# Kernel tuning notes

Measured on AMD Instinct MI355X. Metric: run time of the kernel, lower is better.

Reference implementation:

```python
import jax, jax.numpy as jnp
import numpy as np

D_MODEL = 1024
NUM_HEADS = 16
D_HEAD = D_MODEL // NUM_HEADS
THETA = 10000.0


def _rope_tables(seq_len, d_k, theta):
    # inv_powers_k = theta**(-(2k-2)/d_k) for k=1..d_k/2 == theta**(-arange(0,d_k,2)/d_k)
    inv_powers = theta ** (-jnp.arange(0, d_k, 2, dtype=jnp.float32) / d_k)  # [d_k/2]
    positions = jnp.arange(seq_len, dtype=jnp.float32)
    angles = jnp.outer(positions, inv_powers)  # [S, d_k/2]
    return jnp.cos(angles), jnp.sin(angles)


def _apply_rope(x, cos, sin):
    # x: [..., S, d_k]; cos/sin: [S, d_k/2] broadcast over leading dims
    x_even = x[..., 0::2]
    x_odd = x[..., 1::2]
    r_even = x_even * cos - x_odd * sin
    r_odd = x_even * sin + x_odd * cos
    # interleave back: [..., S, d_k/2, 2] -> [..., S, d_k]
    return jnp.stack([r_even, r_odd], axis=-1).reshape(x.shape)


def setup_inputs() -> dict:
    key = jax.random.key(0)
    ks = jax.random.split(key, 5)
    B, S = 2, 2048
    sigma = (2.0 / (D_MODEL + D_MODEL)) ** 0.5
    x = jax.random.normal(ks[0], (B, S, D_MODEL), dtype=jnp.float32)
    wq = jax.random.normal(ks[1], (D_MODEL, D_MODEL), dtype=jnp.float32) * sigma
    wk = jax.random.normal(ks[2], (D_MODEL, D_MODEL), dtype=jnp.float32) * sigma
    wv = jax.random.normal(ks[3], (D_MODEL, D_MODEL), dtype=jnp.float32) * sigma
    wo = jax.random.normal(ks[4], (D_MODEL, D_MODEL), dtype=jnp.float32) * sigma
    return {"x": x, "wq": wq, "wk": wk, "wv": wv, "wo": wo}


def reference(x, wq, wk, wv, wo):
    B, S, D = x.shape
    H, Dh = NUM_HEADS, D_HEAD
    # Linear: einx.dot('... in, out in -> ... out') == x @ W.T
    q = jnp.einsum('bsd,od->bso', x, wq)
    k = jnp.einsum('bsd,od->bso', x, wk)
    v = jnp.einsum('bsd,od->bso', x, wv)
    # split heads: [B, S, H, Dh] -> [B, H, S, Dh]
    q = q.reshape(B, S, H, Dh).transpose(0, 2, 1, 3)
    k = k.reshape(B, S, H, Dh).transpose(0, 2, 1, 3)
    v = v.reshape(B, S, H, Dh).transpose(0, 2, 1, 3)
    cos, sin = _rope_tables(S, Dh, THETA)
    q = _apply_rope(q, cos, sin)
    k = _apply_rope(k, cos, sin)
    scale = 1.0 / jnp.sqrt(jnp.float32(Dh))
    scores = jnp.einsum('bhqd,bhkd->bhqk', q, k) * scale  # [B,H,S,S]
    causal = jnp.tril(jnp.ones((S, S), dtype=bool))
    scores = jnp.where(causal, scores, -jnp.inf)
    probs = jax.nn.softmax(scores, axis=-1)
    attn = jnp.einsum('bhqk,bhkd->bhqd', probs, v)
    attn = attn.transpose(0, 2, 1, 3).reshape(B, S, D)
    return jnp.einsum('bsd,od->bso', attn, wo)
```

## Files before the change

### kernel.cpp

```cpp
#include <hip/hip_runtime.h>
#include <hip/hip_bf16.h>
#include <math.h>

#define B_SZ   2
#define SEQ    2048
#define DM     1024
#define NH     16
#define DH     64
#define MROWS  (B_SZ * SEQ)
#define DQKV   (3 * DM)

typedef __attribute__((ext_vector_type(8))) short short8;
typedef __attribute__((ext_vector_type(4))) float f32x4;
typedef __attribute__((ext_vector_type(4))) unsigned short us4;
typedef __attribute__((ext_vector_type(2))) unsigned int u32x2;

__device__ __forceinline__ float b2f(unsigned short u) {
    union { float f; unsigned int i; } x; x.i = ((unsigned int)u) << 16; return x.f;
}
__device__ __forceinline__ unsigned short f2b(float f) {
    union { float f; unsigned int i; } x; x.f = f;
    return (unsigned short)((x.i + 0x7fffu + ((x.i >> 16) & 1u)) >> 16);
}
__device__ __forceinline__ unsigned int pk2b(float a, float b) {
    float2 f2; f2.x = a; f2.y = b;
    __hip_bfloat162 hb = __float22bfloat162_rn(f2);
    return *reinterpret_cast<unsigned int*>(&hb);
}

__device__ __forceinline__ void gload_lds16(const unsigned short* g, unsigned short* lds_base_uniform) {
    __builtin_amdgcn_global_load_lds(
        (const __attribute__((address_space(1))) unsigned int*)g,
        (__attribute__((address_space(3))) unsigned int*)lds_base_uniform,
        16, 0, 0);
}

#define NX4 (MROWS * DM / 4)
#define NW4 (DM * DM / 4)

__global__ __launch_bounds__(256) void cvt_all(const float* __restrict__ x,
                                               const float* __restrict__ wq,
                                               const float* __restrict__ wk,
                                               const float* __restrict__ wv,
                                               const float* __restrict__ wo,
                                               unsigned short* __restrict__ xb,
                                               unsigned short* __restrict__ wqkv,
                                               unsigned short* __restrict__ wob,
                                               float* __restrict__ tab) {
    const int i = blockIdx.x * 256 + threadIdx.x;
    const int ncvt = NX4 + 4 * NW4;
    if (i < ncvt) {
        const float* src; unsigned short* dst; int off;
        if (i < NX4) { src = x; dst = xb; off = i; }
        else {
            int j = i - NX4;
            int w = j >> 18;
            off = j & (NW4 - 1);
            src = (w == 0) ? wq : (w == 1) ? wk : (w == 2) ? wv : wo;
            dst = (w < 3) ? wqkv + (size_t)w * DM * DM : wob;
        }
        float4 v = reinterpret_cast<const float4*>(src)[off];
        us4 o = { f2b(v.x), f2b(v.y), f2b(v.z), f2b(v.w) };
        reinterpret_cast<us4*>(dst)[off] = o;
    } else {
        int t = i - ncvt;
        if (t < SEQ * 32) {
            int s = t >> 5, fi = t & 31;
            float inv = powf(10000.0f, -(float)fi / 32.0f);
            float ang = (float)s * inv;
            tab[2 * t]     = cosf(ang);
            tab[2 * t + 1] = sinf(ang);
        }
    }
}

#define BM 128
#define BN 128
#define BK 32

__global__ __launch_bounds__(256, 2) void gemm_out(const unsigned short* __restrict__ A,
                                                   const unsigned short* __restrict__ B,
                                                   float* __restrict__ Cout) {
    const int OBM = 128, OBN = 64;
    __shared__ unsigned short As[2][OBM * BK];
    __shared__ unsigned short Bs[2][OBN * BK];
    const int tid  = threadIdx.x;
    const int lane = tid & 63, wid = tid >> 6;
    const int lm = lane & 15, lg = lane >> 4;
    const int brow = blockIdx.y * OBM, bcol = blockIdx.x * OBN;
    const int K = DM, N = DM;

    f32x4 acc[2][4] = {};

    const int rA  = tid >> 2;
    const int kc8 = (tid & 3) * 8;
    const unsigned short* gA0 = A + (size_t)(brow + rA) * K + kc8;
    const unsigned short* gA1 = A + (size_t)(brow + 64 + rA) * K + kc8;
    const unsigned short* gB0 = B + (size_t)(bcol + rA) * K + kc8;
    unsigned short* lA0 = (unsigned short*)As + wid * 512;
    unsigned short* lA1 = (unsigned short*)As + 2048 + wid * 512;
    unsigned short* lB0 = (unsigned short*)Bs + wid * 512;

    gload_lds16(gA0, lA0);
    gload_lds16(gA1, lA1);
    gload_lds16(gB0, lB0);
    __syncthreads();

    int buf = 0;
    for (int k0 = 0; k0 < K; k0 += BK) {
        if (k0 + BK < K) {
            gload_lds16(gA0 + k0 + BK, lA0 + (buf ^ 1) * 4096);
            gload_lds16(gA1 + k0 + BK, lA1 + (buf ^ 1) * 4096);
            gload_lds16(gB0 + k0 + BK, lB0 + (buf ^ 1) * 2048);
        }
        short8 a[2], b[4];
#pragma unroll
        for (int m = 0; m < 2; ++m)
            a[m] = *reinterpret_cast<const short8*>(&As[buf][(wid * 32 + m * 16 + lm) * BK + lg * 8]);
#pragma unroll
        for (int n = 0; n < 4; ++n)
            b[n] = *reinterpret_cast<const short8*>(&Bs[buf][(n * 16 + lm) * BK + lg * 8]);
#pragma unroll
        for (int m = 0; m < 2; ++m)
#pragma unroll
            for (int n = 0; n < 4; ++n)
                acc[m][n] = __builtin_amdgcn_mfma_f32_16x16x32_bf16(a[m], b[n], acc[m][n], 0, 0, 0);
        __syncthreads();
        buf ^= 1;
    }

#pragma unroll
    for (int m = 0; m < 2; ++m) {
#pragma unroll
        for (int r = 0; r < 4; ++r) {
            const size_t base = (size_t)(brow + wid * 32 + m * 16 + lg * 4 + r) * N + bcol + lm;
#pragma unroll
            for (int n = 0; n < 4; ++n)
                Cout[base + n * 16] = acc[m][n][r];
        }
    }
}

__global__ __launch_bounds__(256, 2) void gemm_qkv(const unsigned short* __restrict__ A,
                                                   const unsigned short* __restrict__ B,
                                                   unsigned short* __restrict__ qkv,
                                                   unsigned short* __restrict__ vT,
                                                   const float* __restrict__ tab) {
    __shared__ unsigned short As[2][BM * BK];
    __shared__ unsigned short Bs[2][BN * BK];
    const int tid  = threadIdx.x;
    const int lane = tid & 63, wid = tid >> 6;
    const int wr = wid >> 1, wc = wid & 1;
    const int lm = lane & 15, lg = lane >> 4;
    const int brow = blockIdx.y * BM, bcol = blockIdx.x * BN;
    const int K = DM;

    f32x4 acc[4][4] = {};

    const int rA  = tid >> 2;
    const int kc8 = (tid & 3) * 8;
    const unsigned short* gA0 = A + (size_t)(brow + rA) * K + kc8;
    const unsigned short* gA1 = A + (size_t)(brow + 64 + rA) * K + kc8;
    const unsigned short* gB0 = B + (size_t)(bcol + rA) * K + kc8;
    const unsigned short* gB1 = B + (size_t)(bcol + 64 + rA) * K + kc8;
    unsigned short* lA0 = (unsigned short*)As + wid * 512;
    unsigned short* lA1 = (unsigned short*)As + 2048 + wid * 512;
    unsigned short* lB0 = (unsigned short*)Bs + wid * 512;
    unsigned short* lB1 = (unsigned short*)Bs + 2048 + wid * 512;

    gload_lds16(gA0, lA0);
    gload_lds16(gA1, lA1);
    gload_lds16(gB0, lB0);
    gload_lds16(gB1, lB1);
    __syncthreads();

    int buf = 0;
    for (int k0 = 0; k0 < K; k0 += BK) {
        if (k0 + BK < K) {
            const int bo = (buf ^ 1) * 4096;
            gload_lds16(gA0 + k0 + BK, lA0 + bo);
            gload_lds16(gA1 + k0 + BK, lA1 + bo);
            gload_lds16(gB0 + k0 + BK, lB0 + bo);
            gload_lds16(gB1 + k0 + BK, lB1 + bo);
        }
        short8 a[4], b[4];
#pragma unroll
        for (int m = 0; m < 4; ++m)
            a[m] = *reinterpret_cast<const short8*>(&As[buf][(wr * 64 + m * 16 + lm) * BK + lg * 8]);
#pragma unroll
        for (int n = 0; n < 4; ++n)
            b[n] = *reinterpret_cast<const short8*>(&Bs[buf][(wc * 64 + n * 16 + lm) * BK + lg * 8]);
#pragma unroll
        for (int m = 0; m < 4; ++m)
#pragma unroll
            for (int n = 0; n < 4; ++n)
                acc[m][n] = __builtin_amdgcn_mfma_f32_16x16x32_bf16(a[m], b[n], acc[m][n], 0, 0, 0);
        __syncthreads();
        buf ^= 1;
    }

    const int reg = blockIdx.x >> 3;
    if (reg < 2) {
        const float qs = (reg == 0) ? (0.125f * 1.4426950408889634f) : 1.0f;
        const int odd = lm & 1;
#pragma unroll
        for (int m = 0; m < 4; ++m) {
#pragma unroll
            for (int r = 0; r < 4; ++r) {
                const int row = brow + wr * 64 + m * 16 + lg * 4 + r;
                const int s   = row & (SEQ - 1);
                const size_t base = (size_t)row * DQKV + bcol + wc * 64 + lm;
#pragma unroll
                for (int n = 0; n < 4; ++n) {
                    float v  = acc[m][n][r];
                    float pv = __shfl_xor(v, 1);
                    const int fi = (n * 16 + lm) >> 1;
                    float2 cs = reinterpret_cast<const float2*>(tab)[s * 32 + fi];
                    float c = cs.x * qs, sn = cs.y * qs;
                    float out = odd ? (pv * sn + v * c) : (v * c - pv * sn);
                    qkv[base + n * 16] = f2b(out);
                }
            }
        }
    } else {
        const int b = brow >> 11;
#pragma unroll
        for (int m = 0; m < 4; ++m) {
            const int s0 = (brow + wr * 64 + m * 16 + lg * 4) & (SEQ - 1);
#pragma unroll
            for (int n = 0; n < 4; ++n) {
                const int vcol = bcol + wc * 64 + n * 16 + lm - 2 * DM;
                const int h = vcol >> 6, d = vcol & 63;
                us4 val = { f2b(acc[m][n][0]), f2b(acc[m][n][1]),
                            f2b(acc[m][n][2]), f2b(acc[m][n][3]) };
                *reinterpret_cast<us4*>(vT + (size_t)((b * NH + h) * DH + d) * SEQ + s0) = val;
            }
        }
    }
}

__global__ __launch_bounds__(256, 2) void attn_mfma(const unsigned short* __restrict__ qkv,
                                                    const unsigned short* __restrict__ vT,
                                                    unsigned short* __restrict__ o) {
    const int tid  = threadIdx.x;
    const int wid  = tid >> 6;
    const int lane = tid & 63;
    const int lm = lane & 15, lg = lane >> 4;

    const int bid = blockIdx.x;
    const int u   = bid >> 3;
    const int bh  = (bid & 7) + 8 * (u >> 4);
    const int c0  = u & 15;
    const int b = bh >> 4, h = bh & 15;

    __shared__ unsigned short Kl[2][4096];
    __shared__ unsigned short Vl[2][4096];
    __shared__ unsigned int   Pex[4][16 * 34];
    unsigned int* PW = Pex[wid];

    const unsigned short* kb = qkv + ((size_t)b * SEQ) * DQKV + DM + h * DH;
    const unsigned short* vb = vT + ((size_t)bh) * DH * SEQ;

    const int rloc = tid >> 3;
    const int cs   = (tid & 7) ^ (rloc & 7);
    const unsigned short* kst0 = kb + (size_t)rloc * DQKV + cs * 8;
    const unsigned short* kst1 = kb + (size_t)(rloc + 32) * DQKV + cs * 8;
    const unsigned short* vst0 = vb + (size_t)rloc * SEQ + cs * 8;
    const unsigned short* vst1 = vb + (size_t)(rloc + 32) * SEQ + cs * 8;
    const int sdst = wid * 512;

    const int sl0  = (lg ^ (lm & 7)) << 4;
    const int sl1  = ((lg + 4) ^ (lm & 7)) << 4;
    const int rowb = lm * 128;

    const int wr_base = lm * 34 + lg * 2;
    const int rd1 = lm * 34 + (lg >> 1) * 8 + (lg & 1) * 4;
    const int rd2 = rd1 + 16;

    for (int half = 0; half < 2; ++half) {
        const int c     = (half == 0) ? (31 - c0) : c0;
        const int qbase = c * 64 + wid * 16;
        const int nb    = c + 1;

        const unsigned short* qrow = qkv + ((size_t)(b * SEQ + qbase + lm)) * DQKV + h * DH;
        short8 qa0 = *reinterpret_cast<const short8*>(qrow + lg * 8);
        short8 qa1 = *reinterpret_cast<const short8*>(qrow + 32 + lg * 8);

        f32x4 o0 = {0.f, 0.f, 0.f, 0.f}, o1 = o0, o2 = o0, o3 = o0;
        float mrun = -INFINITY, lrun = 0.f;

        gload_lds16(kst0, &Kl[0][sdst]);
        gload_lds16(kst1, &Kl[0][2048 + sdst]);
        gload_lds16(vst0, &Vl[0][sdst]);
        gload_lds16(vst1, &Vl[0][2048 + sdst]);
        __syncthreads();

        int buf = 0;
        for (int blk = 0; blk < nb; ++blk) {
            const int kbase = blk << 6;

            if (blk + 1 < nb) {
                const size_t ko = (size_t)(kbase + 64) * DQKV;
                const int    vo = kbase + 64;
                gload_lds16(kst0 + ko, &Kl[buf ^ 1][sdst]);
                gload_lds16(kst1 + ko, &Kl[buf ^ 1][2048 + sdst]);
                gload_lds16(vst0 + vo, &Vl[buf ^ 1][sdst]);
                gload_lds16(vst1 + vo, &Vl[buf ^ 1][2048 + sdst]);
            }

            const char* Kb = (const char*)&Kl[buf][0];
            const char* Vb = (const char*)&Vl[buf][0];

            float s[16];
            __builtin_amdgcn_s_setprio(1);
#pragma unroll
            for (int st = 0; st < 4; ++st) {
                short8 k0 = *reinterpret_cast<const short8*>(Kb + st * 2048 + rowb + sl0);
                short8 k1 = *reinterpret_cast<const short8*>(Kb + st * 2048 + rowb + sl1);
                f32x4 t = {0.f, 0.f, 0.f, 0.f};
                t = __builtin_amdgcn_mfma_f32_16x16x32_bf16(k0, qa0, t, 0, 0, 0);
                t = __builtin_amdgcn_mfma_f32_16x16x32_bf16(k1, qa1, t, 0, 0, 0);
#pragma unroll
                for (int r = 0; r < 4; ++r) s[st * 4 + r] = t[r];
            }
            __builtin_amdgcn_s_setprio(0);

            short8 vf[8];
#pragma unroll
            for (int c4 = 0; c4 < 4; ++c4) {
                vf[c4 * 2]     = *reinterpret_cast<const short8*>(Vb + c4 * 2048 + rowb + sl0);
                vf[c4 * 2 + 1] = *reinterpret_cast<const short8*>(Vb + c4 * 2048 + rowb + sl1);
            }

            if (blk == nb - 1) {
#pragma unroll
                for (int st = 0; st < 4; ++st)
#pragma unroll
                    for (int r = 0; r < 4; ++r) {
                        int kk = kbase + st * 16 + lg * 4 + r;
                        s[st * 4 + r] = (kk <= qbase + lm) ? s[st * 4 + r] : -INFINITY;
                    }
            }

            float t0 = fmaxf(s[0], s[1]),  t1 = fmaxf(s[2], s[3]);
            float t2 = fmaxf(s[4], s[5]),  t3 = fmaxf(s[6], s[7]);
            float t4 = fmaxf(s[8], s[9]),  t5 = fmaxf(s[10], s[11]);
            float t6 = fmaxf(s[12], s[13]), t7 = fmaxf(s[14], s[15]);
            float lmax = fmaxf(fmaxf(fmaxf(t0, t1), fmaxf(t2, t3)),
                               fmaxf(fmaxf(t4, t5), fmaxf(t6, t7)));

            if (!__all(lmax - mrun <= 8.0f)) {
                float mx = lmax;
                mx = fmaxf(mx, __shfl_xor(mx, 16));
                mx = fmaxf(mx, __shfl_xor(mx, 32));
                float mn  = fmaxf(mrun, mx);
                float fsc = exp2f(mrun - mn);
                mrun = mn;
                lrun *= fsc;
                float fr[4];
#pragma unroll
                for (int r = 0; r < 4; ++r) fr[r] = __shfl(fsc, lg * 4 + r);
#pragma unroll
                for (int r = 0; r < 4; ++r) {
                    o0[r] *= fr[r]; o1[r] *= fr[r]; o2[r] *= fr[r]; o3[r] *= fr[r];
                }
            }

#pragma unroll
            for (int i = 0; i < 16; ++i) s[i] = exp2f(s[i] - mrun);
            float a0 = (s[0] + s[1]) + (s[2] + s[3]);
            float a1 = (s[4] + s[5]) + (s[6] + s[7]);
            float a2 = (s[8] + s[9]) + (s[10] + s[11]);
            float a3 = (s[12] + s[13]) + (s[14] + s[15]);
            float ps = (a0 + a1) + (a2 + a3);
            ps += __shfl_xor(ps, 16);
            ps += __shfl_xor(ps, 32);
            lrun += ps;

#pragma unroll
            for (int st = 0; st < 4; ++st) {
                u32x2 w;
                w.x = pk2b(s[st * 4 + 0], s[st * 4 + 1]);
                w.y = pk2b(s[st * 4 + 2], s[st * 4 + 3]);
                *reinterpret_cast<u32x2*>(&PW[wr_base + st * 8]) = w;
            }
            __builtin_amdgcn_wave_barrier();
            asm volatile("" ::: "memory");

            union { unsigned int u[4]; short8 v; } pk1, pk2;
            {
                u32x2 x0 = *reinterpret_cast<const u32x2*>(&PW[rd1]);
                u32x2 x1 = *reinterpret_cast<const u32x2*>(&PW[rd1 + 2]);
                pk1.u[0] = x0.x; pk1.u[1] = x0.y; pk1.u[2] = x1.x; pk1.u[3] = x1.y;
                u32x2 y0 = *reinterpret_cast<const u32x2*>(&PW[rd2]);
                u32x2 y1 = *reinterpret_cast<const u32x2*>(&PW[rd2 + 2]);
                pk2.u[0] = y0.x; pk2.u[1] = y0.y; pk2.u[2] = y1.x; pk2.u[3] = y1.y;
            }
            __builtin_amdgcn_wave_barrier();
            asm volatile("" ::: "memory");

            __builtin_amdgcn_s_setprio(1);
            o0 = __builtin_amdgcn_mfma_f32_16x16x32_bf16(pk1.v, vf[0], o0, 0, 0, 0);
            o0 = __builtin_amdgcn_mfma_f32_16x16x32_bf16(pk2.v, vf[1], o0, 0, 0, 0);
            o1 = __builtin_amdgcn_mfma_f32_16x16x32_bf16(pk1.v, vf[2], o1, 0, 0, 0);
            o1 = __builtin_amdgcn_mfma_f32_16x16x32_bf16(pk2.v, vf[3], o1, 0, 0, 0);
            o2 = __builtin_amdgcn_mfma_f32_16x16x32_bf16(pk1.v, vf[4], o2, 0, 0, 0);
            o2 = __builtin_amdgcn_mfma_f32_16x16x32_bf16(pk2.v, vf[5], o2, 0, 0, 0);
            o3 = __builtin_amdgcn_mfma_f32_16x16x32_bf16(pk1.v, vf[6], o3, 0, 0, 0);
            o3 = __builtin_amdgcn_mfma_f32_16x16x32_bf16(pk2.v, vf[7], o3, 0, 0, 0);
            __builtin_amdgcn_s_setprio(0);

            __syncthreads();
            buf ^= 1;
        }

        float linv[4];
#pragma unroll
        for (int r = 0; r < 4; ++r) linv[r] = 1.0f / __shfl(lrun, lg * 4 + r);
#pragma unroll
        for (int r = 0; r < 4; ++r) {
            const size_t rowoff = ((size_t)(b * SEQ + qbase + lg * 4 + r)) * DM + h * DH;
            o[rowoff + 0 * 16 + lm] = f2b(o0[r] * linv[r]);
            o[rowoff + 1 * 16 + lm] = f2b(o1[r] * linv[r]);
            o[rowoff + 2 * 16 + lm] = f2b(o2[r] * linv[r]);
            o[rowoff + 3 * 16 + lm] = f2b(o3[r] * linv[r]);
        }
    }
}

extern "C" void kernel_launch(void* const* d_in, const int* in_sizes, int n_in,
                              void* d_out, int out_size, void* d_ws, size_t ws_size,
                              hipStream_t stream) {
    const float* x  = (const float*)d_in[0];
    const float* wq = (const float*)d_in[1];
    const float* wk = (const float*)d_in[2];
    const float* wv = (const float*)d_in[3];
    const float* wo = (const float*)d_in[4];
    float* out = (float*)d_out;

    char* ws = (char*)d_ws;
    const size_t MB = 1024 * 1024;
    unsigned short* xb      = (unsigned short*)(ws);
    unsigned short* wqkv    = (unsigned short*)(ws + 8 * MB);
    unsigned short* wob     = (unsigned short*)(ws + 14 * MB);
    unsigned short* qkv     = (unsigned short*)(ws + 16 * MB);
    unsigned short* vT      = (unsigned short*)(ws + 40 * MB);
    float*          ropetab = (float*)(ws + 48 * MB);
    unsigned short* attn_bf = xb;

    const int cvt_grid = (NX4 + 4 * NW4 + SEQ * 32) / 256;
    cvt_all<<<cvt_grid, 256, 0, stream>>>(x, wq, wk, wv, wo, xb, wqkv, wob, ropetab);

    gemm_qkv<<<dim3(DQKV / BN, MROWS / BM), 256, 0, stream>>>(xb, wqkv, qkv, vT, ropetab);

    attn_mfma<<<512, 256, 0, stream>>>(qkv, vT, attn_bf);

    gemm_out<<<dim3(DM / 64, MROWS / 128), 256, 0, stream>>>(attn_bf, wob, out);
}
```

Baseline: 126.1 us.

## Rewrite causal attention with 32x32x16 MFMA tiles and in-register P exchange

The attention kernel moves from 16x16x32 MFMA tiles to 32x32x16 tiles, so each wave now owns 32 query rows and each block owns a 128-row chunk. The old two-half balanced loop over 64-row chunks becomes a single pass, with blocks ordered so heavy and light chunks are mixed. The LDS round-trip that converted P into an MFMA operand is replaced by v_permlane32_swap within registers, and exp2 now uses the raw v_exp_f32 instruction. The aim is fewer LDS accesses and instructions per FLOP. In exchange, accumulator register pressure rises and the last two key blocks of each chunk need masking, which may hurt occupancy or load balance.

```diff
diff --git a/kernel.cpp b/kernel.cpp
--- a/kernel.cpp
+++ b/kernel.cpp
@@ -12,6 +12,7 @@
 
 typedef __attribute__((ext_vector_type(8))) short short8;
 typedef __attribute__((ext_vector_type(4))) float f32x4;
+typedef __attribute__((ext_vector_type(16))) float f32x16;
 typedef __attribute__((ext_vector_type(4))) unsigned short us4;
 typedef __attribute__((ext_vector_type(2))) unsigned int u32x2;
 
@@ -26,6 +27,12 @@
     float2 f2; f2.x = a; f2.y = b;
     __hip_bfloat162 hb = __float22bfloat162_rn(f2);
     return *reinterpret_cast<unsigned int*>(&hb);
+}
+__device__ __forceinline__ float fexp2(float x) {
+    float r; asm("v_exp_f32 %0, %1" : "=v"(r) : "v"(x)); return r;
+}
+__device__ __forceinline__ void swap32(unsigned int& a, unsigned int& b) {
+    asm("v_permlane32_swap_b32 %0, %1" : "+v"(a), "+v"(b));
 }
 
 __device__ __forceinline__ void gload_lds16(const unsigned short* g, unsigned short* lds_base_uniform) {
@@ -81,13 +88,13 @@
 __global__ __launch_bounds__(256, 2) void gemm_out(const unsigned short* __restrict__ A,
                                                    const unsigned short* __restrict__ B,
                                                    float* __restrict__ Cout) {
-    const int OBM = 128, OBN = 64;
+    const int OBM = 128;
     __shared__ unsigned short As[2][OBM * BK];
-    __shared__ unsigned short Bs[2][OBN * BK];
+    __shared__ unsigned short Bs[2][64 * BK];
     const int tid  = threadIdx.x;
     const int lane = tid & 63, wid = tid >> 6;
     const int lm = lane & 15, lg = lane >> 4;
-    const int brow = blockIdx.y * OBM, bcol = blockIdx.x * OBN;
+    const int brow = blockIdx.y * OBM, bcol = blockIdx.x * 64;
     const int K = DM, N = DM;
 
     f32x4 acc[2][4] = {};
@@ -245,18 +252,20 @@
     const int tid  = threadIdx.x;
     const int wid  = tid >> 6;
     const int lane = tid & 63;
-    const int lm = lane & 15, lg = lane >> 4;
+    const int l31 = lane & 31, lo = lane >> 5;
 
     const int bid = blockIdx.x;
     const int u   = bid >> 3;
-    const int bh  = (bid & 7) + 8 * (u >> 4);
-    const int c0  = u & 15;
+    const int j   = u & 31, hi = u >> 5;
+    const int bh_hi = (hi ? 2 : 0) + (j >> 4);
+    const int chunk = hi ? (15 - (j & 15)) : (j & 15);
+    const int bh = (bid & 7) + 8 * bh_hi;
     const int b = bh >> 4, h = bh & 15;
+    const int qbase = chunk * 128 + wid * 32;
+    const int nb = 2 * chunk + 2;
 
     __shared__ unsigned short Kl[2][4096];
     __shared__ unsigned short Vl[2][4096];
-    __shared__ unsigned int   Pex[4][16 * 34];
-    unsigned int* PW = Pex[wid];
 
     const unsigned short* kb = qkv + ((size_t)b * SEQ) * DQKV + DM + h * DH;
     const unsigned short* vb = vT + ((size_t)bh) * DH * SEQ;
@@ -269,162 +278,149 @@
     const unsigned short* vst1 = vb + (size_t)(rloc + 32) * SEQ + cs * 8;
     const int sdst = wid * 512;
 
-    const int sl0  = (lg ^ (lm & 7)) << 4;
-    const int sl1  = ((lg + 4) ^ (lm & 7)) << 4;
-    const int rowb = lm * 128;
-
-    const int wr_base = lm * 34 + lg * 2;
-    const int rd1 = lm * 34 + (lg >> 1) * 8 + (lg & 1) * 4;
-    const int rd2 = rd1 + 16;
-
-    for (int half = 0; half < 2; ++half) {
-        const int c     = (half == 0) ? (31 - c0) : c0;
-        const int qbase = c * 64 + wid * 16;
-        const int nb    = c + 1;
-
-        const unsigned short* qrow = qkv + ((size_t)(b * SEQ + qbase + lm)) * DQKV + h * DH;
-        short8 qa0 = *reinterpret_cast<const short8*>(qrow + lg * 8);
-        short8 qa1 = *reinterpret_cast<const short8*>(qrow + 32 + lg * 8);
-
-        f32x4 o0 = {0.f, 0.f, 0.f, 0.f}, o1 = o0, o2 = o0, o3 = o0;
-        float mrun = -INFINITY, lrun = 0.f;
-
-        gload_lds16(kst0, &Kl[0][sdst]);
-        gload_lds16(kst1, &Kl[0][2048 + sdst]);
-        gload_lds16(vst0, &Vl[0][sdst]);
-        gload_lds16(vst1, &Vl[0][2048 + sdst]);
+    const unsigned short* qr = qkv + ((size_t)(b * SEQ + qbase + l31)) * DQKV + h * DH + lo * 8;
+    short8 qb4[4];
+#pragma unroll
+    for (int dc = 0; dc < 4; ++dc)
+        qb4[dc] = *reinterpret_cast<const short8*>(qr + dc * 16);
+
+    f32x16 oA = {0,0,0,0,0,0,0,0,0,0,0,0,0,0,0,0};
+    f32x16 oB = {0,0,0,0,0,0,0,0,0,0,0,0,0,0,0,0};
+    float mrun = -INFINITY, lrun = 0.f;
+
+    gload_lds16(kst0, &Kl[0][sdst]);
+    gload_lds16(kst1, &Kl[0][2048 + sdst]);
+    gload_lds16(vst0, &Vl[0][sdst]);
+    gload_lds16(vst1, &Vl[0][2048 + sdst]);
+    __syncthreads();
+
+    int buf = 0;
+    for (int blk = 0; blk < nb; ++blk) {
+        const int kbase = blk << 6;
+
+        if (blk + 1 < nb) {
+            const size_t ko = (size_t)(kbase + 64) * DQKV;
+            const int    vo = kbase + 64;
+            gload_lds16(kst0 + ko, &Kl[buf ^ 1][sdst]);
+            gload_lds16(kst1 + ko, &Kl[buf ^ 1][2048 + sdst]);
+            gload_lds16(vst0 + vo, &Vl[buf ^ 1][sdst]);
+            gload_lds16(vst1 + vo, &Vl[buf ^ 1][2048 + sdst]);
+        }
+
+        const char* Kb = (const char*)&Kl[buf][0];
+        const char* Vb = (const char*)&Vl[buf][0];
+
+        f32x16 S0 = {0,0,0,0,0,0,0,0,0,0,0,0,0,0,0,0};
+        f32x16 S1 = {0,0,0,0,0,0,0,0,0,0,0,0,0,0,0,0};
+        __builtin_amdgcn_s_setprio(1);
+#pragma unroll
+        for (int dc = 0; dc < 4; ++dc) {
+            const int slot = dc * 2 + lo;
+            short8 k0 = *reinterpret_cast<const short8*>(Kb + l31 * 128 + ((slot ^ (l31 & 7)) << 4));
+            short8 k1 = *reinterpret_cast<const short8*>(Kb + (32 + l31) * 128 + ((slot ^ (l31 & 7)) << 4));
+            S0 = __builtin_amdgcn_mfma_f32_32x32x16_bf16(k0, qb4[dc], S0, 0, 0, 0);
+            S1 = __builtin_amdgcn_mfma_f32_32x32x16_bf16(k1, qb4[dc], S1, 0, 0, 0);
+        }
+        __builtin_amdgcn_s_setprio(0);
+
+        short8 vf[4][2];
+#pragma unroll
+        for (int kc = 0; kc < 4; ++kc) {
+#pragma unroll
+            for (int dh = 0; dh < 2; ++dh) {
+                const int row = dh * 32 + l31;
+                const int slot = kc * 2 + lo;
+                vf[kc][dh] = *reinterpret_cast<const short8*>(Vb + row * 128 + ((slot ^ (row & 7)) << 4));
+            }
+        }
+
+        float s0[16], s1[16];
+#pragma unroll
+        for (int r = 0; r < 16; ++r) { s0[r] = S0[r]; s1[r] = S1[r]; }
+
+        if (blk + 2 >= nb) {
+            const int q = qbase + l31;
+#pragma unroll
+            for (int r = 0; r < 16; ++r) {
+                const int kk = kbase + (r & 3) + 8 * (r >> 2) + 4 * lo;
+                s0[r] = (kk <= q) ? s0[r] : -INFINITY;
+                s1[r] = (kk + 32 <= q) ? s1[r] : -INFINITY;
+            }
+        }
+
+        float tmax[8];
+#pragma unroll
+        for (int i = 0; i < 8; ++i)
+            tmax[i] = fmaxf(fmaxf(s0[2 * i], s0[2 * i + 1]), fmaxf(s1[2 * i], s1[2 * i + 1]));
+        float lmax = fmaxf(fmaxf(fmaxf(tmax[0], tmax[1]), fmaxf(tmax[2], tmax[3])),
+                           fmaxf(fmaxf(tmax[4], tmax[5]), fmaxf(tmax[6], tmax[7])));
+
+        if (!__all(lmax - mrun <= 8.0f)) {
+            float mx = fmaxf(lmax, __shfl_xor(lmax, 32));
+            float mn = fmaxf(mrun, mx);
+            float fsc = fexp2(mrun - mn);
+            mrun = mn;
+            lrun *= fsc;
+#pragma unroll
+            for (int r = 0; r < 16; ++r) {
+                float fr = __shfl(fsc, (r & 3) + 8 * (r >> 2) + 4 * lo);
+                oA[r] *= fr; oB[r] *= fr;
+            }
+        }
+
+#pragma unroll
+        for (int r = 0; r < 16; ++r) { s0[r] = fexp2(s0[r] - mrun); s1[r] = fexp2(s1[r] - mrun); }
+
+        float ac[8];
+#pragma unroll
+        for (int i = 0; i < 8; ++i)
+            ac[i] = (s0[2 * i] + s0[2 * i + 1]) + (s1[2 * i] + s1[2 * i + 1]);
+        float ps = ((ac[0] + ac[1]) + (ac[2] + ac[3])) + ((ac[4] + ac[5]) + (ac[6] + ac[7]));
+        ps += __shfl_xor(ps, 32);
+        lrun += ps;
+
+        unsigned int pf[4][4];
+#pragma unroll
+        for (int s = 0; s < 2; ++s) {
+            const float* sp = s ? s1 : s0;
+            unsigned int a0 = pk2b(sp[0], sp[1]);
+            unsigned int b0 = pk2b(sp[4], sp[5]);
+            swap32(a0, b0);
+            unsigned int a1 = pk2b(sp[2], sp[3]);
+            unsigned int b1 = pk2b(sp[6], sp[7]);
+            swap32(a1, b1);
+            pf[2 * s][0] = a0; pf[2 * s][1] = a1; pf[2 * s][2] = b0; pf[2 * s][3] = b1;
+            unsigned int a2 = pk2b(sp[8], sp[9]);
+            unsigned int b2 = pk2b(sp[12], sp[13]);
+            swap32(a2, b2);
+            unsigned int a3 = pk2b(sp[10], sp[11]);
+            unsigned int b3 = pk2b(sp[14], sp[15]);
+            swap32(a3, b3);
+            pf[2 * s + 1][0] = a2; pf[2 * s + 1][1] = a3; pf[2 * s + 1][2] = b2; pf[2 * s + 1][3] = b3;
+        }
+
+        __builtin_amdgcn_s_setprio(1);
+#pragma unroll
+        for (int kc = 0; kc < 4; ++kc) {
+            union { unsigned int u[4]; short8 v; } P;
+            P.u[0] = pf[kc][0]; P.u[1] = pf[kc][1]; P.u[2] = pf[kc][2]; P.u[3] = pf[kc][3];
+            oA = __builtin_amdgcn_mfma_f32_32x32x16_bf16(P.v, vf[kc][0], oA, 0, 0, 0);
+            oB = __builtin_amdgcn_mfma_f32_32x32x16_bf16(P.v, vf[kc][1], oB, 0, 0, 0);
+        }
+        __builtin_amdgcn_s_setprio(0);
+
         __syncthreads();
-
-        int buf = 0;
-        for (int blk = 0; blk < nb; ++blk) {
-            const int kbase = blk << 6;
-
-            if (blk + 1 < nb) {
-                const size_t ko = (size_t)(kbase + 64) * DQKV;
-                const int    vo = kbase + 64;
-                gload_lds16(kst0 + ko, &Kl[buf ^ 1][sdst]);
-                gload_lds16(kst1 + ko, &Kl[buf ^ 1][2048 + sdst]);
-                gload_lds16(vst0 + vo, &Vl[buf ^ 1][sdst]);
-                gload_lds16(vst1 + vo, &Vl[buf ^ 1][2048 + sdst]);
-            }
-
-            const char* Kb = (const char*)&Kl[buf][0];
-            const char* Vb = (const char*)&Vl[buf][0];
-
-            float s[16];
-            __builtin_amdgcn_s_setprio(1);
-#pragma unroll
-            for (int st = 0; st < 4; ++st) {
-                short8 k0 = *reinterpret_cast<const short8*>(Kb + st * 2048 + rowb + sl0);
-                short8 k1 = *reinterpret_cast<const short8*>(Kb + st * 2048 + rowb + sl1);
-                f32x4 t = {0.f, 0.f, 0.f, 0.f};
-                t = __builtin_amdgcn_mfma_f32_16x16x32_bf16(k0, qa0, t, 0, 0, 0);
-                t = __builtin_amdgcn_mfma_f32_16x16x32_bf16(k1, qa1, t, 0, 0, 0);
-#pragma unroll
-                for (int r = 0; r < 4; ++r) s[st * 4 + r] = t[r];
-            }
-            __builtin_amdgcn_s_setprio(0);
-
-            short8 vf[8];
-#pragma unroll
-            for (int c4 = 0; c4 < 4; ++c4) {
-                vf[c4 * 2]     = *reinterpret_cast<const short8*>(Vb + c4 * 2048 + rowb + sl0);
-                vf[c4 * 2 + 1] = *reinterpret_cast<const short8*>(Vb + c4 * 2048 + rowb + sl1);
-            }
-
-            if (blk == nb - 1) {
-#pragma unroll
-                for (int st = 0; st < 4; ++st)
-#pragma unroll
-                    for (int r = 0; r < 4; ++r) {
-                        int kk = kbase + st * 16 + lg * 4 + r;
-                        s[st * 4 + r] = (kk <= qbase + lm) ? s[st * 4 + r] : -INFINITY;
-                    }
-            }
-
-            float t0 = fmaxf(s[0], s[1]),  t1 = fmaxf(s[2], s[3]);
-            float t2 = fmaxf(s[4], s[5]),  t3 = fmaxf(s[6], s[7]);
-            float t4 = fmaxf(s[8], s[9]),  t5 = fmaxf(s[10], s[11]);
-            float t6 = fmaxf(s[12], s[13]), t7 = fmaxf(s[14], s[15]);
-            float lmax = fmaxf(fmaxf(fmaxf(t0, t1), fmaxf(t2, t3)),
-                               fmaxf(fmaxf(t4, t5), fmaxf(t6, t7)));
-
-            if (!__all(lmax - mrun <= 8.0f)) {
-                float mx = lmax;
-                mx = fmaxf(mx, __shfl_xor(mx, 16));
-                mx = fmaxf(mx, __shfl_xor(mx, 32));
-                float mn  = fmaxf(mrun, mx);
-                float fsc = exp2f(mrun - mn);
-                mrun = mn;
-                lrun *= fsc;
-                float fr[4];
-#pragma unroll
-                for (int r = 0; r < 4; ++r) fr[r] = __shfl(fsc, lg * 4 + r);
-#pragma unroll
-                for (int r = 0; r < 4; ++r) {
-                    o0[r] *= fr[r]; o1[r] *= fr[r]; o2[r] *= fr[r]; o3[r] *= fr[r];
-                }
-            }
-
-#pragma unroll
-            for (int i = 0; i < 16; ++i) s[i] = exp2f(s[i] - mrun);
-            float a0 = (s[0] + s[1]) + (s[2] + s[3]);
-            float a1 = (s[4] + s[5]) + (s[6] + s[7]);
-            float a2 = (s[8] + s[9]) + (s[10] + s[11]);
-            float a3 = (s[12] + s[13]) + (s[14] + s[15]);
-            float ps = (a0 + a1) + (a2 + a3);
-            ps += __shfl_xor(ps, 16);
-            ps += __shfl_xor(ps, 32);
-            lrun += ps;
-
-#pragma unroll
-            for (int st = 0; st < 4; ++st) {
-                u32x2 w;
-                w.x = pk2b(s[st * 4 + 0], s[st * 4 + 1]);
-                w.y = pk2b(s[st * 4 + 2], s[st * 4 + 3]);
-                *reinterpret_cast<u32x2*>(&PW[wr_base + st * 8]) = w;
-            }
-            __builtin_amdgcn_wave_barrier();
-            asm volatile("" ::: "memory");
-
-            union { unsigned int u[4]; short8 v; } pk1, pk2;
-            {
-                u32x2 x0 = *reinterpret_cast<const u32x2*>(&PW[rd1]);
-                u32x2 x1 = *reinterpret_cast<const u32x2*>(&PW[rd1 + 2]);
-                pk1.u[0] = x0.x; pk1.u[1] = x0.y; pk1.u[2] = x1.x; pk1.u[3] = x1.y;
-                u32x2 y0 = *reinterpret_cast<const u32x2*>(&PW[rd2]);
-                u32x2 y1 = *reinterpret_cast<const u32x2*>(&PW[rd2 + 2]);
-                pk2.u[0] = y0.x; pk2.u[1] = y0.y; pk2.u[2] = y1.x; pk2.u[3] = y1.y;
-            }
-            __builtin_amdgcn_wave_barrier();
-            asm volatile("" ::: "memory");
-
-            __builtin_amdgcn_s_setprio(1);
-            o0 = __builtin_amdgcn_mfma_f32_16x16x32_bf16(pk1.v, vf[0], o0, 0, 0, 0);
-            o0 = __builtin_amdgcn_mfma_f32_16x16x32_bf16(pk2.v, vf[1], o0, 0, 0, 0);
-            o1 = __builtin_amdgcn_mfma_f32_16x16x32_bf16(pk1.v, vf[2], o1, 0, 0, 0);
-            o1 = __builtin_amdgcn_mfma_f32_16x16x32_bf16(pk2.v, vf[3], o1, 0, 0, 0);
-            o2 = __builtin_amdgcn_mfma_f32_16x16x32_bf16(pk1.v, vf[4], o2, 0, 0, 0);
-            o2 = __builtin_amdgcn_mfma_f32_16x16x32_bf16(pk2.v, vf[5], o2, 0, 0, 0);
-            o3 = __builtin_amdgcn_mfma_f32_16x16x32_bf16(pk1.v, vf[6], o3, 0, 0, 0);
-            o3 = __builtin_amdgcn_mfma_f32_16x16x32_bf16(pk2.v, vf[7], o3, 0, 0, 0);
-            __builtin_amdgcn_s_setprio(0);
-
-            __syncthreads();
-            buf ^= 1;
-        }
-
-        float linv[4];
-#pragma unroll
-        for (int r = 0; r < 4; ++r) linv[r] = 1.0f / __shfl(lrun, lg * 4 + r);
-#pragma unroll
-        for (int r = 0; r < 4; ++r) {
-            const size_t rowoff = ((size_t)(b * SEQ + qbase + lg * 4 + r)) * DM + h * DH;
-            o[rowoff + 0 * 16 + lm] = f2b(o0[r] * linv[r]);
-            o[rowoff + 1 * 16 + lm] = f2b(o1[r] * linv[r]);
-            o[rowoff + 2 * 16 + lm] = f2b(o2[r] * linv[r]);
-            o[rowoff + 3 * 16 + lm] = f2b(o3[r] * linv[r]);
-        }
+        buf ^= 1;
+    }
+
+    const float rl = 1.0f / lrun;
+#pragma unroll
+    for (int r = 0; r < 16; ++r) {
+        const int qr = (r & 3) + 8 * (r >> 2) + 4 * lo;
+        const float linv = __shfl(rl, qr);
+        const size_t rowoff = ((size_t)(b * SEQ + qbase + qr)) * DM + h * DH;
+        o[rowoff + l31]      = f2b(oA[r] * linv);
+        o[rowoff + 32 + l31] = f2b(oB[r] * linv);
     }
 }
 
```

New measurement: 122.1 us. -3.2%, faster.
